# Kernel tuning notes

Measured on AMD Instinct MI355X. Metric: run time of the kernel, lower is better.

## Reference

```python
import jax, jax.numpy as jnp
import numpy as np

N_NODES = 50000
N_EDGES = 800000
H = 128
IN_DIM = 512
N_LAYERS = 3
LN_EPS = 1e-5


def setup_inputs() -> dict:
    key = jax.random.key(0)
    ks = jax.random.split(key, 12)
    s_in = 1.0 / np.sqrt(IN_DIM)
    s_h = 1.0 / np.sqrt(H)
    return {
        "peptide_feature": jax.random.normal(ks[0], (N_NODES, IN_DIM), jnp.float32),
        "proj_W": jax.random.uniform(ks[1], (IN_DIM, H), jnp.float32, -s_in, s_in),
        "proj_b": jax.random.uniform(ks[2], (H,), jnp.float32, -s_in, s_in),
        "edge_emb": jax.random.normal(ks[3], (100, H), jnp.float32),
        "conv_W1": jax.random.uniform(ks[4], (N_LAYERS, H, H), jnp.float32, -s_h, s_h),
        "conv_b1": jax.random.uniform(ks[5], (N_LAYERS, H), jnp.float32, -s_h, s_h),
        "conv_W2": jax.random.uniform(ks[6], (N_LAYERS, H, H), jnp.float32, -s_h, s_h),
        "conv_b2": jax.random.uniform(ks[7], (N_LAYERS, H), jnp.float32, -s_h, s_h),
        "ln_gamma": jnp.ones((H,), jnp.float32),
        "ln_beta": jnp.zeros((H,), jnp.float32),
        "edge_index": jax.random.randint(ks[8], (2, N_EDGES), 0, N_NODES, jnp.int64 if jax.config.jax_enable_x64 else jnp.int32),
        "edge_attr": jax.random.randint(ks[9], (N_EDGES, 1), 0, 100, jnp.int64 if jax.config.jax_enable_x64 else jnp.int32),
    }


def reference(peptide_feature, proj_W, proj_b, edge_emb, conv_W1, conv_b1,
              conv_W2, conv_b2, ln_gamma, ln_beta, edge_index, edge_attr):
    # aanet_proj: Linear(512, H)
    x = peptide_feature @ proj_W + proj_b  # [N, H]
    # edge type embedding lookup
    ea = edge_emb[edge_attr[:, 0]]  # [E, H]
    src, dst = edge_index[0], edge_index[1]
    n = x.shape[0]
    for i in range(N_LAYERS):
        # GINEConv (eps=0): aggr_i = sum_{(j->i)} relu(x_j + e_ji); out = MLP(x + aggr)
        msg = jax.nn.relu(x[src] + ea)  # [E, H] gather + add + relu
        agg = jax.ops.segment_sum(msg, dst, num_segments=n)  # scatter-add [N, H]
        h = x + agg
        h = jax.nn.relu(h @ conv_W1[i] + conv_b1[i]) @ conv_W2[i] + conv_b2[i]
        x = h + x  # residual
    # LayerNorm over last dim
    mu = jnp.mean(x, axis=-1, keepdims=True)
    var = jnp.var(x, axis=-1, keepdims=True)
    return ln_gamma * (x - mu) * jax.lax.rsqrt(var + LN_EPS) + ln_beta
```

## Files before the change

### kernel.cpp

```cpp
#include <hip/hip_runtime.h>
#include <hip/hip_bf16.h>

#define N_NODES 50000
#define N_EDGES 800000
#define H 128
#define IN_DIM 512
#define N_LAYERS 3
#define LN_EPS 1e-5f
#define SCAN_B ((N_NODES + 255) / 256)
#define BIN_CH 8192
#define BIN_BLOCKS ((N_EDGES + BIN_CH - 1) / BIN_CH)

typedef __attribute__((ext_vector_type(4))) float f32x4;
typedef __attribute__((ext_vector_type(8))) short short8;

__device__ inline ushort f2bfu(float f) {
    __hip_bfloat16 h = __float2bfloat16(f);
    return __builtin_bit_cast(ushort, h);
}
__device__ inline float bfu2f(ushort u) {
    uint v = ((uint)u) << 16;
    return __builtin_bit_cast(float, v);
}
__device__ inline float lobf(uint u) { return __builtin_bit_cast(float, u << 16); }
__device__ inline float hibf(uint u) { return __builtin_bit_cast(float, u & 0xffff0000u); }

#define SWZ(row, byte) ((byte) ^ (((row) & 7) << 4))

__device__ inline short8 cvt8(float4 a, float4 b) {
    short8 v;
    v[0] = (short)f2bfu(a.x); v[1] = (short)f2bfu(a.y);
    v[2] = (short)f2bfu(a.z); v[3] = (short)f2bfu(a.w);
    v[4] = (short)f2bfu(b.x); v[5] = (short)f2bfu(b.y);
    v[6] = (short)f2bfu(b.z); v[7] = (short)f2bfu(b.w);
    return v;
}


__global__ __launch_bounds__(256) void bucketcnt_k(const int* __restrict__ dst,
                                                   int* __restrict__ bcnt) {
    __shared__ int cnt[SCAN_B];
    int tid = threadIdx.x;
    if (tid < SCAN_B) cnt[tid] = 0;
    __syncthreads();
    int e0 = blockIdx.x * BIN_CH;
    #pragma unroll
    for (int k = 0; k < BIN_CH / 256; k++) {
        int e = e0 + k * 256 + tid;
        if (e < N_EDGES) atomicAdd(&cnt[dst[e] >> 8], 1);
    }
    __syncthreads();
    if (tid < SCAN_B && cnt[tid] > 0) atomicAdd(&bcnt[tid], cnt[tid]);
}

__global__ __launch_bounds__(256) void scanb_k(const int* __restrict__ bcnt,
                                               int* __restrict__ bbase,
                                               int* __restrict__ bcur) {
    __shared__ int s[256];
    int t = threadIdx.x;
    int v = (t < SCAN_B) ? bcnt[t] : 0;
    s[t] = v;
    __syncthreads();
    for (int d = 1; d < 256; d <<= 1) {
        int u = (t >= d) ? s[t - d] : 0;
        __syncthreads();
        s[t] += u;
        __syncthreads();
    }
    int exc = s[t] - v;
    bbase[t] = exc;
    if (t < SCAN_B) bcur[t] = exc;
}

__global__ __launch_bounds__(256) void binpass_k(const int* __restrict__ src,
                                                 const int* __restrict__ dst,
                                                 const int* __restrict__ attr,
                                                 int* __restrict__ bcur,
                                                 int* __restrict__ tmp_ep,
                                                 ushort* __restrict__ tmp_dst) {
    __shared__ int cnt[SCAN_B];
    __shared__ int lofs[SCAN_B];
    __shared__ int gbase[SCAN_B];
    __shared__ int cnt2[SCAN_B];
    __shared__ int scan_s[256];
    __shared__ int stage_ep[BIN_CH];
    __shared__ ushort stage_dst[BIN_CH];
    int tid = threadIdx.x;
    int e0 = blockIdx.x * BIN_CH;

    if (tid < SCAN_B) { cnt[tid] = 0; cnt2[tid] = 0; }
    __syncthreads();

    #pragma unroll
    for (int k = 0; k < BIN_CH / 256; k++) {
        int e = e0 + k * 256 + tid;
        if (e < N_EDGES) atomicAdd(&cnt[dst[e] >> 8], 1);
    }
    __syncthreads();

    int v = (tid < SCAN_B) ? cnt[tid] : 0;
    scan_s[tid] = v;
    __syncthreads();
    for (int d = 1; d < 256; d <<= 1) {
        int u = (tid >= d) ? scan_s[tid - d] : 0;
        __syncthreads();
        scan_s[tid] += u;
        __syncthreads();
    }
    if (tid < SCAN_B) lofs[tid] = scan_s[tid] - v;
    int total = scan_s[255];

    if (tid < SCAN_B && v > 0) gbase[tid] = atomicAdd(&bcur[tid], v);
    __syncthreads();

    #pragma unroll
    for (int k = 0; k < BIN_CH / 256; k++) {
        int e = e0 + k * 256 + tid;
        if (e < N_EDGES) {
            int d = dst[e];
            int b = d >> 8;
            int loc = lofs[b] + atomicAdd(&cnt2[b], 1);
            stage_ep[loc] = src[e] | (attr[e] << 16);
            stage_dst[loc] = (ushort)d;
        }
    }
    __syncthreads();

    for (int i = tid; i < total; i += 256) {
        ushort d = stage_dst[i];
        int b = d >> 8;
        int gp = gbase[b] + (i - lofs[b]);
        tmp_ep[gp] = stage_ep[i];
        tmp_dst[gp] = d;
    }
}

__global__ __launch_bounds__(256) void finepass_k(const int* __restrict__ tmp_ep,
                                                  const ushort* __restrict__ tmp_dst,
                                                  const int* __restrict__ bbase,
                                                  int* __restrict__ offs,
                                                  int* __restrict__ epack) {
    __shared__ int deg[256];
    __shared__ int cur[256];
    __shared__ int wsum[4];
    int tid = threadIdx.x;
    deg[tid] = 0;
    __syncthreads();
    int lo = bbase[blockIdx.x], hi = bbase[blockIdx.x + 1];
    for (int i = lo + tid; i < hi; i += 256)
        atomicAdd(&deg[tmp_dst[i] & 255], 1);
    __syncthreads();
    int lane = tid & 63, w = tid >> 6;
    int v = deg[tid];
    int inc = v;
    #pragma unroll
    for (int d = 1; d < 64; d <<= 1) {
        int u = __shfl_up(inc, d);
        if (lane >= d) inc += u;
    }
    if (lane == 63) wsum[w] = inc;
    __syncthreads();
    int wo = 0;
    #pragma unroll
    for (int k = 0; k < 4; k++) if (k < w) wo += wsum[k];
    int exc = lo + wo + inc - v;
    int node = (blockIdx.x << 8) + tid;
    if (node < N_NODES) offs[node] = exc;
    if (node == N_NODES - 1) offs[N_NODES] = exc + v;
    cur[tid] = exc;
    __syncthreads();
    for (int i = lo + tid; i < hi; i += 256) {
        ushort d = tmp_dst[i];
        int ep = tmp_ep[i];
        int pos = atomicAdd(&cur[d & 255], 1);
        epack[pos] = ep;
    }
}


__global__ __launch_bounds__(256) void prep_w_k(const float* __restrict__ pW,
                                                const float* __restrict__ W1,
                                                const float* __restrict__ W2,
                                                const float* __restrict__ emb,
                                                short* __restrict__ Wt,
                                                short* __restrict__ W1t,
                                                short* __restrict__ W2t,
                                                ushort* __restrict__ embb,
                                                int* __restrict__ bcnt) {
    int i = blockIdx.x * 256 + threadIdx.x;
    if (i < 128 * 512) {
        int n = i >> 9, k = i & 511;
        Wt[i] = (short)f2bfu(pW[k * 128 + n]);
    }
    if (i < 3 * 128 * 128) {
        int l = i >> 14, rem = i & 16383, n = rem >> 7, k = rem & 127;
        W1t[i] = (short)f2bfu(W1[l * 16384 + k * 128 + n]);
        W2t[i] = (short)f2bfu(W2[l * 16384 + k * 128 + n]);
    }
    if (i < 100 * 128) embb[i] = f2bfu(emb[i]);
    if (i < 256) bcnt[i] = 0;
}


__global__ __launch_bounds__(512) void proj_k(const float* __restrict__ pep,
                                              const short* __restrict__ Wt,
                                              const float* __restrict__ b,
                                              float* __restrict__ xf,
                                              ushort* __restrict__ xb) {
    __shared__ short SW[128 * 512];
    int tid = threadIdx.x, lane = tid & 63, wid = tid >> 6;

    #pragma unroll
    for (int c = 0; c < 16; c++) {
        int ch = tid + c * 512;
        int row = ch >> 6, kc = (ch & 63) * 16;
        short8 w = *(const short8*)((const char*)Wt + row * 1024 + kc);
        *(short8*)((char*)SW + SWZ(row, row * 1024 + kc)) = w;
    }
    __syncthreads();

    int m0 = blockIdx.x * 256 + wid * 32;

    const float* arow[2];
    #pragma unroll
    for (int mi = 0; mi < 2; mi++) {
        int node = m0 + mi * 16 + (lane & 15);
        if (node > N_NODES - 1) node = N_NODES - 1;
        arow[mi] = pep + (size_t)node * IN_DIM + ((lane >> 4) << 3);
    }

    f32x4 acc[2][8] = {};
    float4 A[4][2][2];
    #pragma unroll
    for (int d = 0; d < 4; d++)
        #pragma unroll
        for (int mi = 0; mi < 2; mi++) {
            A[d][mi][0] = *(const float4*)(arow[mi] + d * 32);
            A[d][mi][1] = *(const float4*)(arow[mi] + d * 32 + 4);
        }

    #pragma unroll
    for (int ks = 0; ks < 16; ks++) {
        int d = ks & 3;
        short8 af0 = cvt8(A[d][0][0], A[d][0][1]);
        short8 af1 = cvt8(A[d][1][0], A[d][1][1]);
        if (ks + 4 < 16) {
            #pragma unroll
            for (int mi = 0; mi < 2; mi++) {
                A[d][mi][0] = *(const float4*)(arow[mi] + (ks + 4) * 32);
                A[d][mi][1] = *(const float4*)(arow[mi] + (ks + 4) * 32 + 4);
            }
        }
        int kb2 = (ks * 32 + ((lane >> 4) << 3)) * 2;
        #pragma unroll
        for (int ni = 0; ni < 8; ni++) {
            int n = ni * 16 + (lane & 15);
            short8 bf = *(const short8*)((const char*)SW + SWZ(n, n * 1024 + kb2));
            acc[0][ni] = __builtin_amdgcn_mfma_f32_16x16x32_bf16(af0, bf, acc[0][ni], 0, 0, 0);
            acc[1][ni] = __builtin_amdgcn_mfma_f32_16x16x32_bf16(af1, bf, acc[1][ni], 0, 0, 0);
        }
    }

    #pragma unroll
    for (int ni = 0; ni < 8; ni++) {
        int col = ni * 16 + (lane & 15);
        float bb = b[col];
        #pragma unroll
        for (int mi = 0; mi < 2; mi++) {
            int rowb = m0 + mi * 16 + ((lane >> 4) << 2);
            #pragma unroll
            for (int r = 0; r < 4; r++) {
                int node = rowb + r;
                if (node < N_NODES) {
                    float v = acc[mi][ni][r] + bb;
                    xf[(size_t)node * H + col] = v;
                    xb[(size_t)node * H + col] = f2bfu(v);
                }
            }
        }
    }
}


__global__ __launch_bounds__(256) void gather_k(const ushort* __restrict__ xb,
                                                const int* __restrict__ offs,
                                                const int* __restrict__ epack,
                                                const ushort* __restrict__ embb,
                                                ushort* __restrict__ aggb) {
    int node = (blockIdx.x * 256 + threadIdx.x) >> 6;
    int lane = threadIdx.x & 63;
    if (node >= N_NODES) return;
    int beg = offs[node], end = offs[node + 1];
    float ax = 0.f, ay = 0.f;
    for (int base = beg; base < end; base += 64) {
        int myp = (base + lane < end) ? epack[base + lane] : 0;
        int cnt = min(64, end - base);
        int j = 0;
        for (; j + 8 <= cnt; j += 8) {
            int p0 = __shfl(myp, j),     p1 = __shfl(myp, j + 1);
            int p2 = __shfl(myp, j + 2), p3 = __shfl(myp, j + 3);
            int p4 = __shfl(myp, j + 4), p5 = __shfl(myp, j + 5);
            int p6 = __shfl(myp, j + 6), p7 = __shfl(myp, j + 7);
            uint x0 = *(const uint*)(xb + (size_t)(p0 & 0xffff) * H + lane * 2);
            uint e0 = *(const uint*)(embb + (size_t)(p0 >> 16) * H + lane * 2);
            uint x1 = *(const uint*)(xb + (size_t)(p1 & 0xffff) * H + lane * 2);
            uint e1 = *(const uint*)(embb + (size_t)(p1 >> 16) * H + lane * 2);
            uint x2 = *(const uint*)(xb + (size_t)(p2 & 0xffff) * H + lane * 2);
            uint e2 = *(const uint*)(embb + (size_t)(p2 >> 16) * H + lane * 2);
            uint x3 = *(const uint*)(xb + (size_t)(p3 & 0xffff) * H + lane * 2);
            uint e3 = *(const uint*)(embb + (size_t)(p3 >> 16) * H + lane * 2);
            uint x4 = *(const uint*)(xb + (size_t)(p4 & 0xffff) * H + lane * 2);
            uint e4 = *(const uint*)(embb + (size_t)(p4 >> 16) * H + lane * 2);
            uint x5 = *(const uint*)(xb + (size_t)(p5 & 0xffff) * H + lane * 2);
            uint e5 = *(const uint*)(embb + (size_t)(p5 >> 16) * H + lane * 2);
            uint x6 = *(const uint*)(xb + (size_t)(p6 & 0xffff) * H + lane * 2);
            uint e6 = *(const uint*)(embb + (size_t)(p6 >> 16) * H + lane * 2);
            uint x7 = *(const uint*)(xb + (size_t)(p7 & 0xffff) * H + lane * 2);
            uint e7 = *(const uint*)(embb + (size_t)(p7 >> 16) * H + lane * 2);
            ax += fmaxf(lobf(x0) + lobf(e0), 0.f); ay += fmaxf(hibf(x0) + hibf(e0), 0.f);
            ax += fmaxf(lobf(x1) + lobf(e1), 0.f); ay += fmaxf(hibf(x1) + hibf(e1), 0.f);
            ax += fmaxf(lobf(x2) + lobf(e2), 0.f); ay += fmaxf(hibf(x2) + hibf(e2), 0.f);
            ax += fmaxf(lobf(x3) + lobf(e3), 0.f); ay += fmaxf(hibf(x3) + hibf(e3), 0.f);
            ax += fmaxf(lobf(x4) + lobf(e4), 0.f); ay += fmaxf(hibf(x4) + hibf(e4), 0.f);
            ax += fmaxf(lobf(x5) + lobf(e5), 0.f); ay += fmaxf(hibf(x5) + hibf(e5), 0.f);
            ax += fmaxf(lobf(x6) + lobf(e6), 0.f); ay += fmaxf(hibf(x6) + hibf(e6), 0.f);
            ax += fmaxf(lobf(x7) + lobf(e7), 0.f); ay += fmaxf(hibf(x7) + hibf(e7), 0.f);
        }
        for (; j + 4 <= cnt; j += 4) {
            int p0 = __shfl(myp, j), p1 = __shfl(myp, j + 1);
            int p2 = __shfl(myp, j + 2), p3 = __shfl(myp, j + 3);
            uint x0 = *(const uint*)(xb + (size_t)(p0 & 0xffff) * H + lane * 2);
            uint e0 = *(const uint*)(embb + (size_t)(p0 >> 16) * H + lane * 2);
            uint x1 = *(const uint*)(xb + (size_t)(p1 & 0xffff) * H + lane * 2);
            uint e1 = *(const uint*)(embb + (size_t)(p1 >> 16) * H + lane * 2);
            uint x2 = *(const uint*)(xb + (size_t)(p2 & 0xffff) * H + lane * 2);
            uint e2 = *(const uint*)(embb + (size_t)(p2 >> 16) * H + lane * 2);
            uint x3 = *(const uint*)(xb + (size_t)(p3 & 0xffff) * H + lane * 2);
            uint e3 = *(const uint*)(embb + (size_t)(p3 >> 16) * H + lane * 2);
            ax += fmaxf(lobf(x0) + lobf(e0), 0.f); ay += fmaxf(hibf(x0) + hibf(e0), 0.f);
            ax += fmaxf(lobf(x1) + lobf(e1), 0.f); ay += fmaxf(hibf(x1) + hibf(e1), 0.f);
            ax += fmaxf(lobf(x2) + lobf(e2), 0.f); ay += fmaxf(hibf(x2) + hibf(e2), 0.f);
            ax += fmaxf(lobf(x3) + lobf(e3), 0.f); ay += fmaxf(hibf(x3) + hibf(e3), 0.f);
        }
        for (; j < cnt; j++) {
            int p = __shfl(myp, j);
            uint xv = *(const uint*)(xb + (size_t)(p & 0xffff) * H + lane * 2);
            uint ev = *(const uint*)(embb + (size_t)(p >> 16) * H + lane * 2);
            ax += fmaxf(lobf(xv) + lobf(ev), 0.f);
            ay += fmaxf(hibf(xv) + hibf(ev), 0.f);
        }
    }
    uint packed = (uint)f2bfu(ax) | ((uint)f2bfu(ay) << 16);
    *(uint*)(aggb + (size_t)node * H + lane * 2) = packed;
}


#define MLP_ROWS 64
__global__ __launch_bounds__(256) void mlp_k(float* __restrict__ xf,
                                             ushort* __restrict__ xb,
                                             const ushort* __restrict__ aggb,
                                             const short* __restrict__ W1t,
                                             const float* __restrict__ b1,
                                             const short* __restrict__ W2t,
                                             const float* __restrict__ b2,
                                             const float* __restrict__ gamma,
                                             const float* __restrict__ beta,
                                             float* __restrict__ out,
                                             int write_xb, int do_ln) {
    __shared__ short S[MLP_ROWS * 128];
    __shared__ short Wb[128 * 128];
    int tid = threadIdx.x, lane = tid & 63, wid = tid >> 6;
    int wr = wid >> 1, wc = wid & 1;
    int m0 = blockIdx.x * MLP_ROWS;

    #pragma unroll
    for (int c = 0; c < 4; c++) {
        int ch = tid + c * 256;
        int row = ch >> 4, k8 = (ch & 15) * 8;
        int node = m0 + row;
        short8 hv;
        if (node < N_NODES) {
            short8 xv = *(const short8*)(xb + (size_t)node * H + k8);
            short8 ag = *(const short8*)(aggb + (size_t)node * H + k8);
            #pragma unroll
            for (int q = 0; q < 8; q++)
                hv[q] = (short)f2bfu(bfu2f((ushort)xv[q]) + bfu2f((ushort)ag[q]));
        } else {
            hv = (short8)0;
        }
        *(short8*)((char*)S + SWZ(row, row * 256 + k8 * 2)) = hv;
    }
    #pragma unroll
    for (int c = 0; c < 8; c++) {
        int ch = tid + c * 256;
        int row = ch >> 4, k8 = (ch & 15) * 8;
        short8 w = *(const short8*)(W1t + row * H + k8);
        *(short8*)((char*)Wb + SWZ(row, row * 256 + k8 * 2)) = w;
    }
    short8 wreg2[8];
    #pragma unroll
    for (int c = 0; c < 8; c++) {
        int ch = tid + c * 256;
        int row = ch >> 4, k8 = (ch & 15) * 8;
        wreg2[c] = *(const short8*)(W2t + row * H + k8);
    }
    __syncthreads();

    f32x4 a1[2][4] = {};
    #pragma unroll
    for (int ks = 0; ks < 4; ks++) {
        int kb = ks * 32 + (lane >> 4) * 8;
        short8 af[2], bfr[4];
        #pragma unroll
        for (int mi = 0; mi < 2; mi++) {
            int r = wr * 32 + mi * 16 + (lane & 15);
            af[mi] = *(const short8*)((const char*)S + SWZ(r, r * 256 + kb * 2));
        }
        #pragma unroll
        for (int ni = 0; ni < 4; ni++) {
            int n = wc * 64 + ni * 16 + (lane & 15);
            bfr[ni] = *(const short8*)((const char*)Wb + SWZ(n, n * 256 + kb * 2));
        }
        #pragma unroll
        for (int mi = 0; mi < 2; mi++)
            #pragma unroll
            for (int ni = 0; ni < 4; ni++)
                a1[mi][ni] = __builtin_amdgcn_mfma_f32_16x16x32_bf16(
                    af[mi], bfr[ni], a1[mi][ni], 0, 0, 0);
    }
    __syncthreads();

    #pragma unroll
    for (int ni = 0; ni < 4; ni++) {
        int n = wc * 64 + ni * 16 + (lane & 15);
        float bb = b1[n];
        #pragma unroll
        for (int mi = 0; mi < 2; mi++) {
            int mrow = wr * 32 + mi * 16 + ((lane >> 4) << 2);
            #pragma unroll
            for (int r = 0; r < 4; r++) {
                int m = mrow + r;
                float tv = fmaxf(a1[mi][ni][r] + bb, 0.f);
                *(ushort*)((char*)S + SWZ(m, m * 256 + n * 2)) = f2bfu(tv);
            }
        }
    }
    #pragma unroll
    for (int c = 0; c < 8; c++) {
        int ch = tid + c * 256;
        int row = ch >> 4, k8 = (ch & 15) * 8;
        *(short8*)((char*)Wb + SWZ(row, row * 256 + k8 * 2)) = wreg2[c];
    }
    __syncthreads();

    f32x4 a2[4][2] = {};
    #pragma unroll
    for (int ks = 0; ks < 4; ks++) {
        int kb = ks * 32 + (lane >> 4) * 8;
        short8 af[4], bfr[2];
        #pragma unroll
        for (int mi = 0; mi < 4; mi++) {
            int n2 = wr * 64 + mi * 16 + (lane & 15);
            af[mi] = *(const short8*)((const char*)Wb + SWZ(n2, n2 * 256 + kb * 2));
        }
        #pragma unroll
        for (int ni = 0; ni < 2; ni++) {
            int m = wc * 32 + ni * 16 + (lane & 15);
            bfr[ni] = *(const short8*)((const char*)S + SWZ(m, m * 256 + kb * 2));
        }
        #pragma unroll
        for (int mi = 0; mi < 4; mi++)
            #pragma unroll
            for (int ni = 0; ni < 2; ni++)
                a2[mi][ni] = __builtin_amdgcn_mfma_f32_16x16x32_bf16(
                    af[mi], bfr[ni], a2[mi][ni], 0, 0, 0);
    }

    if (!do_ln) {
        #pragma unroll
        for (int ni = 0; ni < 2; ni++) {
            int node = m0 + wc * 32 + ni * 16 + (lane & 15);
            if (node >= N_NODES) continue;
            #pragma unroll
            for (int mi = 0; mi < 4; mi++) {
                int n2b = wr * 64 + mi * 16 + ((lane >> 4) << 2);
                float4 xo = *(float4*)(xf + (size_t)node * H + n2b);
                float4 bb = *(const float4*)(b2 + n2b);
                float4 o;
                o.x = a2[mi][ni][0] + bb.x + xo.x;
                o.y = a2[mi][ni][1] + bb.y + xo.y;
                o.z = a2[mi][ni][2] + bb.z + xo.z;
                o.w = a2[mi][ni][3] + bb.w + xo.w;
                *(float4*)(xf + (size_t)node * H + n2b) = o;
                if (write_xb) {
                    ushort us[4] = {f2bfu(o.x), f2bfu(o.y), f2bfu(o.z), f2bfu(o.w)};
                    *(ulong*)(xb + (size_t)node * H + n2b) = *(ulong*)us;
                }
            }
        }
    } else {
        float* F = (float*)Wb;
        __syncthreads();
        #pragma unroll
        for (int ni = 0; ni < 2; ni++) {
            int nl = wc * 32 + ni * 16 + (lane & 15);
            int node = m0 + nl;
            #pragma unroll
            for (int mi = 0; mi < 4; mi++) {
                int n2b = wr * 64 + mi * 16 + ((lane >> 4) << 2);
                float4 o = {0.f, 0.f, 0.f, 0.f};
                if (node < N_NODES) {
                    float4 xo = *(float4*)(xf + (size_t)node * H + n2b);
                    float4 bb = *(const float4*)(b2 + n2b);
                    o.x = a2[mi][ni][0] + bb.x + xo.x;
                    o.y = a2[mi][ni][1] + bb.y + xo.y;
                    o.z = a2[mi][ni][2] + bb.z + xo.z;
                    o.w = a2[mi][ni][3] + bb.w + xo.w;
                }
                *(float4*)((char*)F + SWZ(nl, nl * 512 + n2b * 4)) = o;
            }
        }
        __syncthreads();
        float2 gm = ((const float2*)gamma)[lane];
        float2 bt = ((const float2*)beta)[lane];
        for (int i = 0; i < 16; i++) {
            int row = wid * 16 + i;
            int node = m0 + row;
            if (node >= N_NODES) break;
            float2 v = *(float2*)((char*)F + SWZ(row, row * 512 + lane * 8));
            float s = v.x + v.y;
            #pragma unroll
            for (int d = 1; d < 64; d <<= 1) s += __shfl_xor(s, d);
            float mu = s * (1.f / 128.f);
            float dx = v.x - mu, dy = v.y - mu;
            float q = dx * dx + dy * dy;
            #pragma unroll
            for (int d = 1; d < 64; d <<= 1) q += __shfl_xor(q, d);
            float inv = rsqrtf(q * (1.f / 128.f) + LN_EPS);
            float2 o2;
            o2.x = gm.x * dx * inv + bt.x;
            o2.y = gm.y * dy * inv + bt.y;
            ((float2*)(out + (size_t)node * H))[lane] = o2;
        }
    }
}


extern "C" void kernel_launch(void* const* d_in, const int* in_sizes, int n_in,
                              void* d_out, int out_size, void* d_ws, size_t ws_size,
                              hipStream_t stream) {
    const float* pep    = (const float*)d_in[0];
    const float* proj_W = (const float*)d_in[1];
    const float* proj_b = (const float*)d_in[2];
    const float* emb    = (const float*)d_in[3];
    const float* cW1    = (const float*)d_in[4];
    const float* cb1    = (const float*)d_in[5];
    const float* cW2    = (const float*)d_in[6];
    const float* cb2    = (const float*)d_in[7];
    const float* gamma  = (const float*)d_in[8];
    const float* beta   = (const float*)d_in[9];
    const int*   eidx   = (const int*)d_in[10];
    const int*   attr   = (const int*)d_in[11];
    const int* src = eidx;
    const int* dst = eidx + N_EDGES;

    char* w = (char*)d_ws;
    float*  xf     = (float*)w;             w += (size_t)N_NODES * H * 4;
    ushort* xb     = (ushort*)w;            w += (size_t)N_NODES * H * 2;
    ushort* aggb   = (ushort*)w;            w += (size_t)N_NODES * H * 2;
    short*  Wt     = (short*)w;             w += 128 * 512 * 2;
    short*  W1t    = (short*)w;             w += 3 * 128 * 128 * 2;
    short*  W2t    = (short*)w;             w += 3 * 128 * 128 * 2;
    ushort* embb   = (ushort*)w;            w += 100 * 128 * 2;
    int*    offs   = (int*)w;               w += (N_NODES + 16) * 4;
    int*    bcnt   = (int*)w;               w += 256 * 4;
    int*    bbase  = (int*)w;               w += 260 * 4;
    int*    bcur   = (int*)w;               w += 256 * 4;
    int*    epack  = (int*)w;               w += (size_t)N_EDGES * 4;
    int*    tmp_ep = (int*)w;               w += (size_t)N_EDGES * 4;
    ushort* tmp_dst = (ushort*)w;           w += (size_t)N_EDGES * 2;

    float* out = (float*)d_out;

    prep_w_k<<<256, 256, 0, stream>>>(proj_W, cW1, cW2, emb, Wt, W1t, W2t, embb, bcnt);
    bucketcnt_k<<<BIN_BLOCKS, 256, 0, stream>>>(dst, bcnt);
    scanb_k<<<1, 256, 0, stream>>>(bcnt, bbase, bcur);
    binpass_k<<<BIN_BLOCKS, 256, 0, stream>>>(src, dst, attr, bcur, tmp_ep, tmp_dst);
    finepass_k<<<SCAN_B, 256, 0, stream>>>(tmp_ep, tmp_dst, bbase, offs, epack);

    proj_k<<<(N_NODES + 255) / 256, 512, 0, stream>>>(pep, Wt, proj_b, xf, xb);

    for (int l = 0; l < N_LAYERS; l++) {
        gather_k<<<(N_NODES * 64 + 255) / 256, 256, 0, stream>>>(
            xb, offs, epack, embb, aggb);
        mlp_k<<<(N_NODES + MLP_ROWS - 1) / MLP_ROWS, 256, 0, stream>>>(
            xf, xb, aggb,
            W1t + (size_t)l * H * H, cb1 + (size_t)l * H,
            W2t + (size_t)l * H * H, cb2 + (size_t)l * H,
            gamma, beta, out,
            (l < N_LAYERS - 1) ? 1 : 0,
            (l == N_LAYERS - 1) ? 1 : 0);
    }
}
```

Measured before the change: 271.7 us.

## Drop fp32 node-state buffer and fuse edge bucket counting into weight prep

Removes the fp32 copy of node features and keeps only the bf16 state, so the residual add reads and writes bf16 in the MLP kernel and the projection writes only bf16. Separately, bucket counting moves into the weight-prep kernel, writing per-block partial counts that the scan kernel sums, which removes one launch and the global atomics. This cuts memory traffic per layer and launch overhead, but the residual stream now accumulates in bf16, which adds rounding error across layers.

```diff
diff --git a/kernel.cpp b/kernel.cpp
--- a/kernel.cpp
+++ b/kernel.cpp
@@ -37,28 +37,52 @@
 }
 
 
-__global__ __launch_bounds__(256) void bucketcnt_k(const int* __restrict__ dst,
-                                                   int* __restrict__ bcnt) {
+__global__ __launch_bounds__(256) void prep_w_k(const float* __restrict__ pW,
+                                                const float* __restrict__ W1,
+                                                const float* __restrict__ W2,
+                                                const float* __restrict__ emb,
+                                                const int* __restrict__ dst,
+                                                short* __restrict__ Wt,
+                                                short* __restrict__ W1t,
+                                                short* __restrict__ W2t,
+                                                ushort* __restrict__ embb,
+                                                int* __restrict__ bcnt_part) {
     __shared__ int cnt[SCAN_B];
-    int tid = threadIdx.x;
-    if (tid < SCAN_B) cnt[tid] = 0;
-    __syncthreads();
-    int e0 = blockIdx.x * BIN_CH;
-    #pragma unroll
-    for (int k = 0; k < BIN_CH / 256; k++) {
-        int e = e0 + k * 256 + tid;
-        if (e < N_EDGES) atomicAdd(&cnt[dst[e] >> 8], 1);
-    }
-    __syncthreads();
-    if (tid < SCAN_B && cnt[tid] > 0) atomicAdd(&bcnt[tid], cnt[tid]);
-}
-
-__global__ __launch_bounds__(256) void scanb_k(const int* __restrict__ bcnt,
+    int tid = threadIdx.x, bid = blockIdx.x;
+    int i = bid * 256 + tid;
+    if (i < 128 * 512) {
+        int n = i >> 9, k = i & 511;
+        Wt[i] = (short)f2bfu(pW[k * 128 + n]);
+    }
+    if (i < 3 * 128 * 128) {
+        int l = i >> 14, rem = i & 16383, n = rem >> 7, k = rem & 127;
+        W1t[i] = (short)f2bfu(W1[l * 16384 + k * 128 + n]);
+        W2t[i] = (short)f2bfu(W2[l * 16384 + k * 128 + n]);
+    }
+    if (i < 100 * 128) embb[i] = f2bfu(emb[i]);
+
+    if (bid < BIN_BLOCKS) {
+        if (tid < SCAN_B) cnt[tid] = 0;
+        __syncthreads();
+        int e0 = bid * BIN_CH;
+        #pragma unroll
+        for (int k = 0; k < BIN_CH / 256; k++) {
+            int e = e0 + k * 256 + tid;
+            if (e < N_EDGES) atomicAdd(&cnt[dst[e] >> 8], 1);
+        }
+        __syncthreads();
+        if (tid < SCAN_B) bcnt_part[bid * SCAN_B + tid] = cnt[tid];
+    }
+}
+
+__global__ __launch_bounds__(256) void scanb_k(const int* __restrict__ bcnt_part,
                                                int* __restrict__ bbase,
                                                int* __restrict__ bcur) {
     __shared__ int s[256];
     int t = threadIdx.x;
-    int v = (t < SCAN_B) ? bcnt[t] : 0;
+    int v = 0;
+    if (t < SCAN_B)
+        for (int b = 0; b < BIN_BLOCKS; b++) v += bcnt_part[b * SCAN_B + t];
     s[t] = v;
     __syncthreads();
     for (int d = 1; d < 256; d <<= 1) {
@@ -178,34 +202,9 @@
 }
 
 
-__global__ __launch_bounds__(256) void prep_w_k(const float* __restrict__ pW,
-                                                const float* __restrict__ W1,
-                                                const float* __restrict__ W2,
-                                                const float* __restrict__ emb,
-                                                short* __restrict__ Wt,
-                                                short* __restrict__ W1t,
-                                                short* __restrict__ W2t,
-                                                ushort* __restrict__ embb,
-                                                int* __restrict__ bcnt) {
-    int i = blockIdx.x * 256 + threadIdx.x;
-    if (i < 128 * 512) {
-        int n = i >> 9, k = i & 511;
-        Wt[i] = (short)f2bfu(pW[k * 128 + n]);
-    }
-    if (i < 3 * 128 * 128) {
-        int l = i >> 14, rem = i & 16383, n = rem >> 7, k = rem & 127;
-        W1t[i] = (short)f2bfu(W1[l * 16384 + k * 128 + n]);
-        W2t[i] = (short)f2bfu(W2[l * 16384 + k * 128 + n]);
-    }
-    if (i < 100 * 128) embb[i] = f2bfu(emb[i]);
-    if (i < 256) bcnt[i] = 0;
-}
-
-
 __global__ __launch_bounds__(512) void proj_k(const float* __restrict__ pep,
                                               const short* __restrict__ Wt,
                                               const float* __restrict__ b,
-                                              float* __restrict__ xf,
                                               ushort* __restrict__ xb) {
     __shared__ short SW[128 * 512];
     int tid = threadIdx.x, lane = tid & 63, wid = tid >> 6;
@@ -271,11 +270,8 @@
             #pragma unroll
             for (int r = 0; r < 4; r++) {
                 int node = rowb + r;
-                if (node < N_NODES) {
-                    float v = acc[mi][ni][r] + bb;
-                    xf[(size_t)node * H + col] = v;
-                    xb[(size_t)node * H + col] = f2bfu(v);
-                }
+                if (node < N_NODES)
+                    xb[(size_t)node * H + col] = f2bfu(acc[mi][ni][r] + bb);
             }
         }
     }
@@ -356,8 +352,7 @@
 
 
 #define MLP_ROWS 64
-__global__ __launch_bounds__(256) void mlp_k(float* __restrict__ xf,
-                                             ushort* __restrict__ xb,
+__global__ __launch_bounds__(256) void mlp_k(ushort* __restrict__ xb,
                                              const ushort* __restrict__ aggb,
                                              const short* __restrict__ W1t,
                                              const float* __restrict__ b1,
@@ -366,7 +361,7 @@
                                              const float* __restrict__ gamma,
                                              const float* __restrict__ beta,
                                              float* __restrict__ out,
-                                             int write_xb, int do_ln) {
+                                             int do_ln) {
     __shared__ short S[MLP_ROWS * 128];
     __shared__ short Wb[128 * 128];
     int tid = threadIdx.x, lane = tid & 63, wid = tid >> 6;
@@ -484,18 +479,15 @@
             #pragma unroll
             for (int mi = 0; mi < 4; mi++) {
                 int n2b = wr * 64 + mi * 16 + ((lane >> 4) << 2);
-                float4 xo = *(float4*)(xf + (size_t)node * H + n2b);
+                ulong xr = *(const ulong*)(xb + (size_t)node * H + n2b);
+                const ushort* xp = (const ushort*)&xr;
                 float4 bb = *(const float4*)(b2 + n2b);
-                float4 o;
-                o.x = a2[mi][ni][0] + bb.x + xo.x;
-                o.y = a2[mi][ni][1] + bb.y + xo.y;
-                o.z = a2[mi][ni][2] + bb.z + xo.z;
-                o.w = a2[mi][ni][3] + bb.w + xo.w;
-                *(float4*)(xf + (size_t)node * H + n2b) = o;
-                if (write_xb) {
-                    ushort us[4] = {f2bfu(o.x), f2bfu(o.y), f2bfu(o.z), f2bfu(o.w)};
-                    *(ulong*)(xb + (size_t)node * H + n2b) = *(ulong*)us;
-                }
+                ushort us[4];
+                us[0] = f2bfu(a2[mi][ni][0] + bb.x + bfu2f(xp[0]));
+                us[1] = f2bfu(a2[mi][ni][1] + bb.y + bfu2f(xp[1]));
+                us[2] = f2bfu(a2[mi][ni][2] + bb.z + bfu2f(xp[2]));
+                us[3] = f2bfu(a2[mi][ni][3] + bb.w + bfu2f(xp[3]));
+                *(ulong*)(xb + (size_t)node * H + n2b) = *(ulong*)us;
             }
         }
     } else {
@@ -510,12 +502,13 @@
                 int n2b = wr * 64 + mi * 16 + ((lane >> 4) << 2);
                 float4 o = {0.f, 0.f, 0.f, 0.f};
                 if (node < N_NODES) {
-                    float4 xo = *(float4*)(xf + (size_t)node * H + n2b);
+                    ulong xr = *(const ulong*)(xb + (size_t)node * H + n2b);
+                    const ushort* xp = (const ushort*)&xr;
                     float4 bb = *(const float4*)(b2 + n2b);
-                    o.x = a2[mi][ni][0] + bb.x + xo.x;
-                    o.y = a2[mi][ni][1] + bb.y + xo.y;
-                    o.z = a2[mi][ni][2] + bb.z + xo.z;
-                    o.w = a2[mi][ni][3] + bb.w + xo.w;
+                    o.x = a2[mi][ni][0] + bb.x + bfu2f(xp[0]);
+                    o.y = a2[mi][ni][1] + bb.y + bfu2f(xp[1]);
+                    o.z = a2[mi][ni][2] + bb.z + bfu2f(xp[2]);
+                    o.w = a2[mi][ni][3] + bb.w + bfu2f(xp[3]);
                 }
                 *(float4*)((char*)F + SWZ(nl, nl * 512 + n2b * 4)) = o;
             }
@@ -565,7 +558,6 @@
     const int* dst = eidx + N_EDGES;
 
     char* w = (char*)d_ws;
-    float*  xf     = (float*)w;             w += (size_t)N_NODES * H * 4;
     ushort* xb     = (ushort*)w;            w += (size_t)N_NODES * H * 2;
     ushort* aggb   = (ushort*)w;            w += (size_t)N_NODES * H * 2;
     short*  Wt     = (short*)w;             w += 128 * 512 * 2;
@@ -573,7 +565,7 @@
     short*  W2t    = (short*)w;             w += 3 * 128 * 128 * 2;
     ushort* embb   = (ushort*)w;            w += 100 * 128 * 2;
     int*    offs   = (int*)w;               w += (N_NODES + 16) * 4;
-    int*    bcnt   = (int*)w;               w += 256 * 4;
+    int*    bcnt_part = (int*)w;            w += (size_t)BIN_BLOCKS * SCAN_B * 4;
     int*    bbase  = (int*)w;               w += 260 * 4;
     int*    bcur   = (int*)w;               w += 256 * 4;
     int*    epack  = (int*)w;               w += (size_t)N_EDGES * 4;
@@ -582,23 +574,22 @@
 
     float* out = (float*)d_out;
 
-    prep_w_k<<<256, 256, 0, stream>>>(proj_W, cW1, cW2, emb, Wt, W1t, W2t, embb, bcnt);
-    bucketcnt_k<<<BIN_BLOCKS, 256, 0, stream>>>(dst, bcnt);
-    scanb_k<<<1, 256, 0, stream>>>(bcnt, bbase, bcur);
+    prep_w_k<<<256, 256, 0, stream>>>(proj_W, cW1, cW2, emb, dst,
+                                      Wt, W1t, W2t, embb, bcnt_part);
+    scanb_k<<<1, 256, 0, stream>>>(bcnt_part, bbase, bcur);
     binpass_k<<<BIN_BLOCKS, 256, 0, stream>>>(src, dst, attr, bcur, tmp_ep, tmp_dst);
     finepass_k<<<SCAN_B, 256, 0, stream>>>(tmp_ep, tmp_dst, bbase, offs, epack);
 
-    proj_k<<<(N_NODES + 255) / 256, 512, 0, stream>>>(pep, Wt, proj_b, xf, xb);
+    proj_k<<<(N_NODES + 255) / 256, 512, 0, stream>>>(pep, Wt, proj_b, xb);
 
     for (int l = 0; l < N_LAYERS; l++) {
         gather_k<<<(N_NODES * 64 + 255) / 256, 256, 0, stream>>>(
             xb, offs, epack, embb, aggb);
         mlp_k<<<(N_NODES + MLP_ROWS - 1) / MLP_ROWS, 256, 0, stream>>>(
-            xf, xb, aggb,
+            xb, aggb,
             W1t + (size_t)l * H * H, cb1 + (size_t)l * H,
             W2t + (size_t)l * H * H, cb2 + (size_t)l * H,
             gamma, beta, out,
-            (l < N_LAYERS - 1) ? 1 : 0,
             (l == N_LAYERS - 1) ? 1 : 0);
     }
 }
```

Measured after the change: 256.0 us. 5.8% less time.
